# Optimization experiments

Hardware: AMD Instinct MI355X
Metric: run time of the kernel (lower is better)

The kernel has to match this reference:

```python
import jax, jax.numpy as jnp
import numpy as np
import itertools
from jax import lax

B, F, T = 4096, 10, 480
NW, W = 24, 20          # 24 windows of width 20 (index_list = [0,20,...,480])
HID = 64                 # GRU hidden size
NLAYERS = 2
PAIRS = np.array(list(itertools.combinations(range(F), 2)))  # [45,2]
P = PAIRS.shape[0]
D_IN = 2 * P + 12 * F    # GRU input size = 210
BN_EPS = 1e-5


def setup_inputs() -> dict:
    key = jax.random.key(0)
    ks = jax.random.split(key, 16)
    s = 0.1
    g = 1.0 / np.sqrt(HID)
    inp = {
        "data": jax.random.normal(ks[0], (B, 1, F, T), jnp.float32),
        "conv_w": 1.0 + s * jax.random.normal(ks[1], (), jnp.float32),
        "conv_b": s * jax.random.normal(ks[2], (), jnp.float32),
        "bn_gamma": 1.0 + s * jax.random.normal(ks[3], (14,), jnp.float32),
        "bn_beta": s * jax.random.normal(ks[4], (14,), jnp.float32),
        "gru_Wih0": g * jax.random.normal(ks[5], (3 * HID, D_IN), jnp.float32),
        "gru_Whh0": g * jax.random.normal(ks[6], (3 * HID, HID), jnp.float32),
        "gru_bih0": g * jax.random.normal(ks[7], (3 * HID,), jnp.float32),
        "gru_bhh0": g * jax.random.normal(ks[8], (3 * HID,), jnp.float32),
        "gru_Wih1": g * jax.random.normal(ks[9], (3 * HID, HID), jnp.float32),
        "gru_Whh1": g * jax.random.normal(ks[10], (3 * HID, HID), jnp.float32),
        "gru_bih1": g * jax.random.normal(ks[11], (3 * HID,), jnp.float32),
        "gru_bhh1": g * jax.random.normal(ks[12], (3 * HID,), jnp.float32),
        "comb_a": jnp.asarray(PAIRS[:, 0], jnp.int32),
        "comb_b": jnp.asarray(PAIRS[:, 1], jnp.int32),
    }
    return inp


def _gru_layer(x_seq, Wih, Whh, bih, bhh):
    # x_seq: [B, S, D]
    b = x_seq.shape[0]
    h0 = jnp.zeros((b, HID), x_seq.dtype)

    def step(h, xt):
        gi = xt @ Wih.T + bih           # [B, 3H]
        gh = h @ Whh.T + bhh
        i_r, i_z, i_n = jnp.split(gi, 3, axis=-1)
        h_r, h_z, h_n = jnp.split(gh, 3, axis=-1)
        r = jax.nn.sigmoid(i_r + h_r)
        z = jax.nn.sigmoid(i_z + h_z)
        n = jnp.tanh(i_n + r * h_n)
        h_new = (1.0 - z) * n + z * h
        return h_new, h_new

    hT, ys = lax.scan(step, h0, jnp.swapaxes(x_seq, 0, 1))
    return jnp.swapaxes(ys, 0, 1), hT


def reference(data, conv_w, conv_b, bn_gamma, bn_beta,
              gru_Wih0, gru_Whh0, gru_bih0, gru_bhh0,
              gru_Wih1, gru_Whh1, gru_bih1, gru_bhh1,
              comb_a, comb_b):
    b = data.shape[0]
    # uniform index_list -> reshape time into [NW, W] windows
    x = data[:, 0].reshape(b, F, NW, W)            # [B, F, NW, W]
    mean = x.mean(-1)                              # [B, F, NW]
    cen = x - mean[..., None]
    var = (cen * cen).mean(-1)                     # population var (np.std default)
    std = jnp.sqrt(var)
    m3 = (cen ** 3).mean(-1)
    m4 = (cen ** 4).mean(-1)

    # pairwise cov / corr over feature combinations
    xa = x[:, comb_a]                              # [B, P, NW, W]
    xb = x[:, comb_b]
    ca = xa - mean[:, comb_a][..., None]
    cb = xb - mean[:, comb_b][..., None]
    cov = (ca * cb).sum(-1) / (W - 1)              # [B, P, NW]
    corr = cov / (std[:, comb_a] * std[:, comb_b] + 0.01)

    dec_w = (jnp.arange(1, W + 1, dtype=x.dtype) / (W * (W + 1) / 2.0))
    stats = [
        corr,                                      # 1 ts_corr
        cov,                                       # 2 ts_cov
        std,                                       # 3 ts_stddev
        mean / (std + 0.01),                       # 4 ts_zscore
        x[..., -1] / (x[..., 0] + 0.01) - 1.0,     # 5 ts_return
        (x * dec_w).sum(-1),                       # 6 ts_decaylinear
        mean,                                      # 7 ts_mean
        x.min(-1),                                 # 8 ts_min
        var,                                       # 9 ts_var
        x.sum(-1),                                 # 10 ts_sum
        jnp.median(x, axis=-1),                    # 11 ts_median
        m3 / (std ** 3 + 0.01),                    # 12 ts_skew
        m4 / (std ** 4 + 0.01) - 3.0,              # 13 ts_kurtosis
        x.sum(-1),                                 # 14 ts_sum (again)
    ]

    # 1x1 conv (scalar affine, shared) + per-stat BatchNorm2d(1) in training mode
    outs = []
    for i, s_ in enumerate(stats):
        y = conv_w * s_ + conv_b
        m = y.mean()
        v = y.var()
        outs.append(bn_gamma[i] * (y - m) * lax.rsqrt(v + BN_EPS) + bn_beta[i])
    feat = jnp.concatenate(outs, axis=1)           # [B, D_IN, NW]
    seq = jnp.swapaxes(feat, 1, 2)                 # [B, NW, D_IN]

    ys0, _ = _gru_layer(seq, gru_Wih0, gru_Whh0, gru_bih0, gru_bhh0)
    _, h1 = _gru_layer(ys0, gru_Wih1, gru_Whh1, gru_bih1, gru_bhh1)
    return h1                                      # [B, HID]
```

## Files before the change

kernel.cpp:

```cpp
#include <hip/hip_runtime.h>
#include <math.h>

#define NF 10
#define TLEN 480
#define NWIN 24
#define WLEN 20
#define HID 64
#define NPAIR 45
#define DIN 210
#define NG 14
#define GATES 192
#define NGRP 256
#define FROW 212
#define XROW 484
#define NW1 16384
#define NW2 16384

typedef __attribute__((ext_vector_type(8))) short bf16x8;
typedef __attribute__((ext_vector_type(4))) float f32x4;

#define MFMA(a,b,c) __builtin_amdgcn_mfma_f32_16x16x32_bf16((a),(b),(c),0,0,0)

__device__ __forceinline__ int grp_of(int k){ return (k < 90) ? (k / 45) : 2 + (k - 90) / 10; }

__device__ __forceinline__ void split2(float x, short& hi, short& lo){
    unsigned u = __float_as_uint(x);
    hi = (short)(u >> 16);
    float hf = __uint_as_float(u & 0xffff0000u);
    lo = (short)(__float_as_uint(x - hf) >> 16);
}
__device__ __forceinline__ short bf16rne(float x){
    unsigned u = __float_as_uint(x);
    u += 0x7fffu + ((u >> 16) & 1u);
    return (short)(u >> 16);
}
__device__ __forceinline__ float sigm(float x){
    return __builtin_amdgcn_rcpf(1.f + __builtin_amdgcn_exp2f(x * -1.4426950408889634f));
}
__device__ __forceinline__ float tanhfast(float x){
    return 1.f - 2.f * __builtin_amdgcn_rcpf(1.f + __builtin_amdgcn_exp2f(x * 2.8853900817779268f));
}

__global__ __launch_bounds__(256)
void stats_kernel(const float* __restrict__ data, float* __restrict__ feat32,
                  float* __restrict__ part1, float* __restrict__ part2)
{
    __shared__ __align__(16) float xs[NF * XROW];
    __shared__ float ts[NWIN][121];
    __shared__ float tpdot[NWIN][48];
    __shared__ int ca_s[NPAIR], cb_s[NPAIR];
    int b = blockIdx.x, tid = threadIdx.x;
    const float* src = data + (size_t)b * (NF * TLEN);

    for (int q = tid; q < 1200; q += 256){
        int f = q / 120, r = q % 120;
        *(float4*)&xs[f * XROW + r * 4] = *(const float4*)&src[q * 4];
    }
    if (tid < NPAIR){
        int fa = 0, rem = tid;
        while (rem >= 9 - fa){ rem -= (9 - fa); ++fa; }
        ca_s[tid] = fa; cb_s[tid] = fa + 1 + rem;
    }
    __syncthreads();

    float val[12];
    #pragma unroll
    for (int j = 0; j < 12; ++j) val[j] = 0.f;

    if (tid < 240){
        int f = tid / NWIN, t = tid % NWIN;
        const float* p = &xs[f * XROW + t * WLEN];
        float v[WLEN];
        {
            float4 a0 = *(const float4*)(p + 0);
            float4 a1 = *(const float4*)(p + 4);
            float4 a2 = *(const float4*)(p + 8);
            float4 a3 = *(const float4*)(p + 12);
            float4 a4 = *(const float4*)(p + 16);
            v[0]=a0.x; v[1]=a0.y; v[2]=a0.z; v[3]=a0.w;
            v[4]=a1.x; v[5]=a1.y; v[6]=a1.z; v[7]=a1.w;
            v[8]=a2.x; v[9]=a2.y; v[10]=a2.z; v[11]=a2.w;
            v[12]=a3.x; v[13]=a3.y; v[14]=a3.z; v[15]=a3.w;
            v[16]=a4.x; v[17]=a4.y; v[18]=a4.z; v[19]=a4.w;
        }
        float sum = 0.f, wsum = 0.f;
        #pragma unroll
        for (int i = 0; i < WLEN; ++i){
            sum += v[i];
            wsum += v[i] * ((float)(i + 1) * (1.0f / 210.0f));
        }
        float mean = sum * (1.0f / WLEN);
        float var = 0.f, m3 = 0.f, m4 = 0.f;
        #pragma unroll
        for (int i = 0; i < WLEN; ++i){
            float c = v[i] - mean, c2 = c * c;
            var += c2; m3 += c2 * c; m4 += c2 * c2;
        }
        var *= 0.05f; m3 *= 0.05f; m4 *= 0.05f;
        float sd = sqrtf(var);
        float ratio = v[WLEN - 1] / (v[0] + 0.01f) - 1.0f;

        #pragma unroll
        for (int rr = 0; rr < 10; ++rr){
            #pragma unroll
            for (int i = (rr & 1); i + 1 < 10; i += 2){
                float lo0 = fminf(v[i], v[i + 1]);
                float hi0 = fmaxf(v[i], v[i + 1]);
                v[i] = lo0; v[i + 1] = hi0;
                float lo1 = fminf(v[10 + i], v[10 + i + 1]);
                float hi1 = fmaxf(v[10 + i], v[10 + i + 1]);
                v[10 + i] = lo1; v[10 + i + 1] = hi1;
            }
        }
        float Lmax = fminf(v[0], v[19]);
        float Hmin = fmaxf(v[0], v[19]);
        #pragma unroll
        for (int i = 1; i < 10; ++i){
            float li = fminf(v[i], v[19 - i]);
            float hi2 = fmaxf(v[i], v[19 - i]);
            Lmax = fmaxf(Lmax, li);
            Hmin = fminf(Hmin, hi2);
        }
        float median = 0.5f * (Lmax + Hmin);
        float minv = fminf(v[0], v[10]);
        float s3 = sd * sd * sd;
        float mos = mean / (sd + 0.01f);
        float skew = m3 / (s3 + 0.01f);
        float kurt = m4 / (s3 * sd + 0.01f) - 3.0f;

        val[0]=sd; val[1]=mos; val[2]=ratio; val[3]=wsum; val[4]=mean; val[5]=minv;
        val[6]=var; val[7]=sum; val[8]=median; val[9]=skew; val[10]=kurt; val[11]=sum;
        #pragma unroll
        for (int j = 0; j < 12; ++j) ts[t][j * 10 + f] = val[j];
    }
    {
        int wid = b * 4 + (tid >> 6);
        int lane = tid & 63;
        #pragma unroll
        for (int j = 0; j < 12; ++j){
            float a = val[j], q = val[j] * val[j];
            #pragma unroll
            for (int m = 1; m < 64; m <<= 1){
                a += __shfl_xor(a, m);
                q += __shfl_xor(q, m);
            }
            if (lane == 0){
                part1[(size_t)(2 * j) * NW1 + wid] = a;
                part1[(size_t)(2 * j + 1) * NW1 + wid] = q;
            }
        }
    }

    {
        int w = tid >> 6, l = tid & 63;
        int f = l & 15, kb = l >> 4;
        #pragma unroll 1
        for (int s = 0; s < 6; ++s){
            int nw = w * 6 + s;
            float vv[8];
            #pragma unroll
            for (int j = 0; j < 8; ++j) vv[j] = 0.f;
            if (f < NF && kb < 3){
                const float* p = &xs[f * XROW + nw * WLEN + kb * 8];
                float4 u0 = *(const float4*)p;
                vv[0] = u0.x; vv[1] = u0.y; vv[2] = u0.z; vv[3] = u0.w;
                if (kb < 2){
                    float4 u1 = *(const float4*)(p + 4);
                    vv[4] = u1.x; vv[5] = u1.y; vv[6] = u1.z; vv[7] = u1.w;
                }
            }
            bf16x8 Fh, Fl;
            #pragma unroll
            for (int j = 0; j < 8; ++j){ short hi, lo; split2(vv[j], hi, lo); Fh[j] = hi; Fl[j] = lo; }
            f32x4 g = {0.f, 0.f, 0.f, 0.f};
            g = MFMA(Fh, Fh, g);
            g = MFMA(Fh, Fl, g);
            g = MFMA(Fl, Fh, g);
            #pragma unroll
            for (int i = 0; i < 4; ++i){
                int fa = kb * 4 + i, fb = f;
                if (fa < fb && fb < NF){
                    int pi = (((19 - fa) * fa) >> 1) + fb - fa - 1;
                    tpdot[nw][pi] = g[i];
                }
            }
        }
    }
    __syncthreads();

    size_t grp = b >> 4, e = b & 15;
    {
        float cs = 0.f, cq = 0.f, vs2 = 0.f, vq = 0.f;
        for (int q = tid; q < NWIN * NPAIR; q += 256){
            int t = q / NPAIR, pi = q % NPAIR;
            int fa = ca_s[pi], fb = cb_s[pi];
            float dot = tpdot[t][pi];
            float ma = ts[t][40 + fa], mb = ts[t][40 + fb];
            float sa = ts[t][0 + fa],  sb = ts[t][0 + fb];
            float cov = (dot - (float)WLEN * ma * mb) * (1.0f / (WLEN - 1));
            float corr = cov / (sa * sb + 0.01f);
            size_t base = ((grp * NWIN + t) * 16 + e) * FROW;
            feat32[base + pi] = corr;
            feat32[base + NPAIR + pi] = cov;
            cs += corr; cq += corr * corr;
            vs2 += cov; vq += cov * cov;
        }
        float acc[4] = {cs, cq, vs2, vq};
        int wid = b * 4 + (tid >> 6);
        int lane = tid & 63;
        #pragma unroll
        for (int j = 0; j < 4; ++j){
            float a = acc[j];
            #pragma unroll
            for (int m = 1; m < 64; m <<= 1) a += __shfl_xor(a, m);
            if (lane == 0) part2[(size_t)j * NW2 + wid] = a;
        }
    }
    for (int q = tid; q < NWIN * 120; q += 256){
        int t = q / 120, c = q % 120;
        size_t base = ((grp * NWIN + t) * 16 + e) * FROW;
        feat32[base + 90 + c] = ts[t][c];
    }
    if (tid < 48){
        int t = tid >> 1;
        size_t base = ((grp * NWIN + t) * 16 + e) * FROW;
        feat32[base + 210 + (tid & 1)] = 0.f;
    }
}

__global__ __launch_bounds__(256)
void reduce_kernel(const float* __restrict__ part1, const float* __restrict__ part2,
                   float* __restrict__ accum)
{
    __shared__ float red[256];
    int j = blockIdx.x;
    int g = j % NG, which = j / NG;
    const float* base; int n;
    if (g < 2){ base = part2 + (size_t)(g * 2 + which) * NW2; n = NW2; }
    else      { base = part1 + (size_t)((g - 2) * 2 + which) * NW1; n = NW1; }
    int tid = threadIdx.x;
    float s = 0.f;
    for (int i = tid; i < n; i += 256) s += base[i];
    red[tid] = s; __syncthreads();
    for (int step = 128; step > 0; step >>= 1){
        if (tid < step) red[tid] += red[tid + step];
        __syncthreads();
    }
    if (tid == 0) accum[which * NG + g] = red[0];
}

__global__ __launch_bounds__(256)
void prep_kernel(const float* __restrict__ Wih0, const float* __restrict__ Whh0,
                 const float* __restrict__ Wih1, const float* __restrict__ Whh1,
                 const float* __restrict__ bih0, const float* __restrict__ accum,
                 const float* __restrict__ conv_w, const float* __restrict__ bn_gamma,
                 const float* __restrict__ bn_beta,
                 short* __restrict__ WHh, short* __restrict__ W0h, float* __restrict__ bf0)
{
    __shared__ float scs[NG], shs[NG];
    int tid = threadIdx.x;
    if (tid < NG){
        float N = (tid < 2) ? 4096.f * NPAIR * NWIN : 4096.f * NF * NWIN;
        float m = accum[tid] / N;
        float v = accum[NG + tid] / N - m * m;
        float cw = conv_w[0];
        float A = bn_gamma[tid] * rsqrtf(cw * cw * v + 1e-5f);
        scs[tid] = A * cw;
        shs[tid] = bn_beta[tid] - A * cw * m;
    }
    __syncthreads();
    const int NH = 3 * 2 * 12 * 64 * 8;
    const int N0 = 7 * 12 * 64 * 8;
    for (int i = blockIdx.x * 256 + tid; i < NH + N0; i += gridDim.x * 256){
        if (i < NH){
            int j = i & 7, lane = (i >> 3) & 63, rest = i >> 9;
            int ct = rest % 12; rest /= 12;
            int ks = rest & 1, m = rest >> 1;
            int gg = ct * 16 + (lane & 15);
            int k = ks * 32 + ((lane >> 4) << 3) + j;
            const float* Wm = (m == 0) ? Whh0 : (m == 1) ? Wih1 : Whh1;
            WHh[i] = bf16rne(Wm[gg * HID + k]);
        } else {
            int e2 = i - NH;
            int j = e2 & 7, lane = (e2 >> 3) & 63, rest = e2 >> 9;
            int ct = rest % 12, ks = rest / 12;
            int gg = ct * 16 + (lane & 15);
            int k = ks * 32 + ((lane >> 4) << 3) + j;
            float v = (k < DIN) ? Wih0[gg * DIN + k] * scs[grp_of(k)] : 0.f;
            W0h[e2] = bf16rne(v);
        }
    }
    if (blockIdx.x == 0 && tid < GATES){
        float s = bih0[tid];
        for (int k = 0; k < DIN; ++k) s += Wih0[tid * DIN + k] * shs[grp_of(k)];
        bf0[tid] = s;
    }
}

__device__ __forceinline__ void stage_fa(short (*fab)[64][8], int tix,
                                         const float* __restrict__ feat32, int ht)
{
    for (int q = ht; q < 448; q += 256){
        int c = q >> 4, e = q & 15;
        float vv[8];
        const float* src = &feat32[((size_t)tix * 16 + e) * FROW + c * 8];
        if (c < 26){
            float4 u0 = *(const float4*)src, u1 = *(const float4*)(src + 4);
            vv[0]=u0.x; vv[1]=u0.y; vv[2]=u0.z; vv[3]=u0.w;
            vv[4]=u1.x; vv[5]=u1.y; vv[6]=u1.z; vv[7]=u1.w;
        } else if (c == 26){
            float4 u0 = *(const float4*)src;
            vv[0]=u0.x; vv[1]=u0.y; vv[2]=u0.z; vv[3]=u0.w;
            vv[4]=0.f; vv[5]=0.f; vv[6]=0.f; vv[7]=0.f;
        } else {
            #pragma unroll
            for (int j = 0; j < 8; ++j) vv[j] = 0.f;
        }
        bf16x8 h8, l8;
        #pragma unroll
        for (int j = 0; j < 8; ++j){ short hi, lo; split2(vv[j], hi, lo); h8[j] = hi; l8[j] = lo; }
        *(bf16x8*)&fab[(c >> 2) * 2 + 0][e + 16 * (c & 3)][0] = h8;
        *(bf16x8*)&fab[(c >> 2) * 2 + 1][e + 16 * (c & 3)][0] = l8;
    }
}

__global__ __launch_bounds__(512, 1)
void rec_kernel(const float* __restrict__ feat32,
                const short* __restrict__ WHh, const short* __restrict__ W0h,
                const float* __restrict__ bf0, const float* __restrict__ bhh0,
                const float* __restrict__ bih1, const float* __restrict__ bhh1,
                float* __restrict__ out)
{
    __shared__ __align__(16) short fa[2][14][64][8];
    __shared__ __align__(16) short hp0[2][2][16][72];
    __shared__ __align__(16) short hp1[2][2][16][72];
    int tid = threadIdx.x;
    int w = tid >> 6, l = tid & 63;
    int lm = l & 15, kb = l >> 4;
    int blk = blockIdx.x;

    for (int i = tid; i < 2 * 2 * 16 * 72; i += 512){
        ((short*)hp0)[i] = 0;
        ((short*)hp1)[i] = 0;
    }
    for (int q = tid; q < 448; q += 512){
        int c = q >> 4, e = q & 15;
        float vv[8];
        const float* src = &feat32[((size_t)(blk * NWIN) * 16 + e) * FROW + c * 8];
        if (c < 26){
            float4 u0 = *(const float4*)src, u1 = *(const float4*)(src + 4);
            vv[0]=u0.x; vv[1]=u0.y; vv[2]=u0.z; vv[3]=u0.w;
            vv[4]=u1.x; vv[5]=u1.y; vv[6]=u1.z; vv[7]=u1.w;
        } else if (c == 26){
            float4 u0 = *(const float4*)src;
            vv[0]=u0.x; vv[1]=u0.y; vv[2]=u0.z; vv[3]=u0.w;
            vv[4]=0.f; vv[5]=0.f; vv[6]=0.f; vv[7]=0.f;
        } else {
            #pragma unroll
            for (int j = 0; j < 8; ++j) vv[j] = 0.f;
        }
        bf16x8 h8, l8;
        #pragma unroll
        for (int j = 0; j < 8; ++j){ short hi, lo; split2(vv[j], hi, lo); h8[j] = hi; l8[j] = lo; }
        *(bf16x8*)&fa[0][(c >> 2) * 2 + 0][e + 16 * (c & 3)][0] = h8;
        *(bf16x8*)&fa[0][(c >> 2) * 2 + 1][e + 16 * (c & 3)][0] = l8;
    }

    if (w < 4){
        int jc = w * 16 + lm;
        bf16x8 WH0_[2][3];
        #pragma unroll
        for (int ks = 0; ks < 2; ++ks)
            #pragma unroll
            for (int ro = 0; ro < 3; ++ro)
                WH0_[ks][ro] = *(const bf16x8*)&WHh[((((0 * 2 + ks) * 12) + (ro * 4 + w)) * 64 + l) * 8];
        bf16x8 W0_[7][3];
        #pragma unroll
        for (int ks = 0; ks < 7; ++ks)
            #pragma unroll
            for (int ro = 0; ro < 3; ++ro)
                W0_[ks][ro] = *(const bf16x8*)&W0h[(((ks * 12) + (ro * 4 + w)) * 64 + l) * 8];

        float cr0 = bf0[jc]       + bhh0[jc];
        float cz0 = bf0[jc + 64]  + bhh0[jc + 64];
        float cin0 = bf0[jc + 128];
        float chn0 = bhh0[jc + 128];
        float h0p[4] = {0.f, 0.f, 0.f, 0.f};

        __syncthreads();
        #pragma unroll 1
        for (int k = 0; k < 25; ++k){
            if (k < 24){
                int rb = (k & 1) ^ 1, wb = k & 1;
                bf16x8 h0h[2], h0l[2];
                #pragma unroll
                for (int ks = 0; ks < 2; ++ks){
                    int off = ks * 32 + kb * 8;
                    h0h[ks] = *(const bf16x8*)&hp0[rb][0][lm][off];
                    h0l[ks] = *(const bf16x8*)&hp0[rb][1][lm][off];
                }
                f32x4 ar0 = {cr0, cr0, cr0, cr0};
                f32x4 az0 = {cz0, cz0, cz0, cz0};
                f32x4 ain0 = {cin0, cin0, cin0, cin0};
                f32x4 ahn0 = {chn0, chn0, chn0, chn0};
                #pragma unroll
                for (int ks = 0; ks < 2; ++ks){
                    ar0 = MFMA(h0h[ks], WH0_[ks][0], ar0);  ar0 = MFMA(h0l[ks], WH0_[ks][0], ar0);
                    az0 = MFMA(h0h[ks], WH0_[ks][1], az0);  az0 = MFMA(h0l[ks], WH0_[ks][1], az0);
                    ahn0 = MFMA(h0h[ks], WH0_[ks][2], ahn0); ahn0 = MFMA(h0l[ks], WH0_[ks][2], ahn0);
                }
                #pragma unroll
                for (int ks = 0; ks < 7; ++ks){
                    bf16x8 Fh = *(const bf16x8*)&fa[k & 1][ks * 2 + 0][l][0];
                    bf16x8 Fl = *(const bf16x8*)&fa[k & 1][ks * 2 + 1][l][0];
                    ar0 = MFMA(Fh, W0_[ks][0], ar0);  ar0 = MFMA(Fl, W0_[ks][0], ar0);
                    az0 = MFMA(Fh, W0_[ks][1], az0);  az0 = MFMA(Fl, W0_[ks][1], az0);
                    ain0 = MFMA(Fh, W0_[ks][2], ain0); ain0 = MFMA(Fl, W0_[ks][2], ain0);
                }
                #pragma unroll
                for (int i = 0; i < 4; ++i){
                    int row = kb * 4 + i;
                    float rg = sigm(ar0[i]);
                    float zg = sigm(az0[i]);
                    float nn = tanhfast(ain0[i] + rg * ahn0[i]);
                    float h = (1.f - zg) * nn + zg * h0p[i];
                    h0p[i] = h;
                    short hi, lo; split2(h, hi, lo);
                    hp0[wb][0][row][jc] = hi;
                    hp0[wb][1][row][jc] = lo;
                }
            }
            __syncthreads();
        }
    } else {
        int w2 = w - 4;
        int jc = w2 * 16 + lm;
        int ht = tid - 256;
        bf16x8 WH1_[2][3], WH2_[2][3];
        #pragma unroll
        for (int ks = 0; ks < 2; ++ks)
            #pragma unroll
            for (int ro = 0; ro < 3; ++ro){
                WH1_[ks][ro] = *(const bf16x8*)&WHh[((((1 * 2 + ks) * 12) + (ro * 4 + w2)) * 64 + l) * 8];
                WH2_[ks][ro] = *(const bf16x8*)&WHh[((((2 * 2 + ks) * 12) + (ro * 4 + w2)) * 64 + l) * 8];
            }
        float cr1 = bih1[jc]      + bhh1[jc];
        float cz1 = bih1[jc + 64] + bhh1[jc + 64];
        float cin1 = bih1[jc + 128];
        float chn1 = bhh1[jc + 128];
        float h1p[4] = {0.f, 0.f, 0.f, 0.f};

        __syncthreads();
        #pragma unroll 1
        for (int k = 0; k < 25; ++k){
            if (k < 23) stage_fa(fa[(k + 1) & 1], blk * NWIN + k + 1, feat32, ht);
            if (k >= 1){
                int t = k - 1;
                int rb0 = t & 1;
                int rh = (k & 1) ^ 1, wh = k & 1;
                bf16x8 n0h[2], n0l[2], h1h[2], h1l[2];
                #pragma unroll
                for (int ks = 0; ks < 2; ++ks){
                    int off = ks * 32 + kb * 8;
                    n0h[ks] = *(const bf16x8*)&hp0[rb0][0][lm][off];
                    n0l[ks] = *(const bf16x8*)&hp0[rb0][1][lm][off];
                    h1h[ks] = *(const bf16x8*)&hp1[rh][0][lm][off];
                    h1l[ks] = *(const bf16x8*)&hp1[rh][1][lm][off];
                }
                f32x4 ar1 = {cr1, cr1, cr1, cr1};
                f32x4 az1 = {cz1, cz1, cz1, cz1};
                f32x4 ain1 = {cin1, cin1, cin1, cin1};
                f32x4 ahn1 = {chn1, chn1, chn1, chn1};
                #pragma unroll
                for (int ks = 0; ks < 2; ++ks){
                    ar1 = MFMA(n0h[ks], WH1_[ks][0], ar1);  ar1 = MFMA(n0l[ks], WH1_[ks][0], ar1);
                    az1 = MFMA(n0h[ks], WH1_[ks][1], az1);  az1 = MFMA(n0l[ks], WH1_[ks][1], az1);
                    ain1 = MFMA(n0h[ks], WH1_[ks][2], ain1); ain1 = MFMA(n0l[ks], WH1_[ks][2], ain1);
                    ar1 = MFMA(h1h[ks], WH2_[ks][0], ar1);  ar1 = MFMA(h1l[ks], WH2_[ks][0], ar1);
                    az1 = MFMA(h1h[ks], WH2_[ks][1], az1);  az1 = MFMA(h1l[ks], WH2_[ks][1], az1);
                    ahn1 = MFMA(h1h[ks], WH2_[ks][2], ahn1); ahn1 = MFMA(h1l[ks], WH2_[ks][2], ahn1);
                }
                #pragma unroll
                for (int i = 0; i < 4; ++i){
                    int row = kb * 4 + i;
                    float rg = sigm(ar1[i]);
                    float zg = sigm(az1[i]);
                    float nn = tanhfast(ain1[i] + rg * ahn1[i]);
                    float h = (1.f - zg) * nn + zg * h1p[i];
                    h1p[i] = h;
                    short hi, lo; split2(h, hi, lo);
                    hp1[wh][0][row][jc] = hi;
                    hp1[wh][1][row][jc] = lo;
                }
            }
            __syncthreads();
        }
        #pragma unroll
        for (int i = 0; i < 4; ++i)
            out[((size_t)(blk * 16) + kb * 4 + i) * HID + jc] = h1p[i];
    }
}

extern "C" void kernel_launch(void* const* d_in, const int* in_sizes, int n_in,
                              void* d_out, int out_size, void* d_ws, size_t ws_size,
                              hipStream_t stream) {
    const float* data     = (const float*)d_in[0];
    const float* conv_w   = (const float*)d_in[1];
    const float* bn_gamma = (const float*)d_in[3];
    const float* bn_beta  = (const float*)d_in[4];
    const float* Wih0     = (const float*)d_in[5];
    const float* Whh0     = (const float*)d_in[6];
    const float* bih0     = (const float*)d_in[7];
    const float* bhh0     = (const float*)d_in[8];
    const float* Wih1     = (const float*)d_in[9];
    const float* Whh1     = (const float*)d_in[10];
    const float* bih1     = (const float*)d_in[11];
    const float* bhh1     = (const float*)d_in[12];
    float* out = (float*)d_out;

    char* ws = (char*)d_ws;
    const size_t feat32_bytes = (size_t)NGRP * NWIN * 16 * FROW * 4;
    const size_t WH_BYTES = 3 * 2 * 12 * 64 * 8 * 2;
    const size_t W0_BYTES = 7 * 12 * 64 * 8 * 2;
    const size_t P1_BYTES = (size_t)24 * NW1 * 4;

    float* feat32 = (float*)ws;
    short* WHh  = (short*)(ws + feat32_bytes);
    short* W0h  = (short*)(ws + feat32_bytes + WH_BYTES);
    float* bf0  = (float*)(ws + feat32_bytes + WH_BYTES + W0_BYTES);
    float* accum = (float*)(ws + feat32_bytes + WH_BYTES + W0_BYTES + 1024);
    float* part1 = (float*)(ws + feat32_bytes + WH_BYTES + W0_BYTES + 2048);
    float* part2 = (float*)(ws + feat32_bytes + WH_BYTES + W0_BYTES + 2048 + P1_BYTES);

    stats_kernel<<<4096, 256, 0, stream>>>(data, feat32, part1, part2);
    reduce_kernel<<<28, 256, 0, stream>>>(part1, part2, accum);
    prep_kernel<<<64, 256, 0, stream>>>(Wih0, Whh0, Wih1, Whh1, bih0, accum,
                                        conv_w, bn_gamma, bn_beta, WHh, W0h, bf0);
    rec_kernel<<<NGRP, 512, 0, stream>>>(feat32, WHh, W0h, bf0,
                                         bhh0, bih1, bhh1, out);
}
```

Before: 142.9 us.

## Fuse correlation epilogue into MFMA loop and compute per-block stat sums from shared memory

The pairwise dot products from the MFMA are turned into cov/corr directly in registers and written to global memory, which drops the tpdot shared buffer, the pair index tables and one barrier. The per-stat BN partial sums no longer use 12 wavefront shuffle reductions of 24 values each. Instead 120 threads sum columns of the shared stats table and combine them with shared atomics, giving one partial per block rather than one per wave, so the reduce kernel reads less data. In exchange the corr/cov global writes become more scattered (only the lanes holding valid pairs write) and shared-memory atomics are added.

```diff
diff --git a/kernel.cpp b/kernel.cpp
--- a/kernel.cpp
+++ b/kernel.cpp
@@ -13,7 +13,7 @@
 #define NGRP 256
 #define FROW 212
 #define XROW 484
-#define NW1 16384
+#define NB 4096
 #define NW2 16384
 
 typedef __attribute__((ext_vector_type(8))) short bf16x8;
@@ -47,8 +47,7 @@
 {
     __shared__ __align__(16) float xs[NF * XROW];
     __shared__ float ts[NWIN][121];
-    __shared__ float tpdot[NWIN][48];
-    __shared__ int ca_s[NPAIR], cb_s[NPAIR];
+    __shared__ float sgs[NG], sgq[NG];
     int b = blockIdx.x, tid = threadIdx.x;
     const float* src = data + (size_t)b * (NF * TLEN);
 
@@ -56,16 +55,8 @@
         int f = q / 120, r = q % 120;
         *(float4*)&xs[f * XROW + r * 4] = *(const float4*)&src[q * 4];
     }
-    if (tid < NPAIR){
-        int fa = 0, rem = tid;
-        while (rem >= 9 - fa){ rem -= (9 - fa); ++fa; }
-        ca_s[tid] = fa; cb_s[tid] = fa + 1 + rem;
-    }
+    if (tid < NG){ sgs[tid] = 0.f; sgq[tid] = 0.f; }
     __syncthreads();
-
-    float val[12];
-    #pragma unroll
-    for (int j = 0; j < 12; ++j) val[j] = 0.f;
 
     if (tid < 240){
         int f = tid / NWIN, t = tid % NWIN;
@@ -128,32 +119,27 @@
         float skew = m3 / (s3 + 0.01f);
         float kurt = m4 / (s3 * sd + 0.01f) - 3.0f;
 
-        val[0]=sd; val[1]=mos; val[2]=ratio; val[3]=wsum; val[4]=mean; val[5]=minv;
-        val[6]=var; val[7]=sum; val[8]=median; val[9]=skew; val[10]=kurt; val[11]=sum;
-        #pragma unroll
-        for (int j = 0; j < 12; ++j) ts[t][j * 10 + f] = val[j];
-    }
-    {
-        int wid = b * 4 + (tid >> 6);
-        int lane = tid & 63;
-        #pragma unroll
-        for (int j = 0; j < 12; ++j){
-            float a = val[j], q = val[j] * val[j];
-            #pragma unroll
-            for (int m = 1; m < 64; m <<= 1){
-                a += __shfl_xor(a, m);
-                q += __shfl_xor(q, m);
-            }
-            if (lane == 0){
-                part1[(size_t)(2 * j) * NW1 + wid] = a;
-                part1[(size_t)(2 * j + 1) * NW1 + wid] = q;
-            }
-        }
-    }
+        ts[t][  0 + f] = sd;
+        ts[t][ 10 + f] = mos;
+        ts[t][ 20 + f] = ratio;
+        ts[t][ 30 + f] = wsum;
+        ts[t][ 40 + f] = mean;
+        ts[t][ 50 + f] = minv;
+        ts[t][ 60 + f] = var;
+        ts[t][ 70 + f] = sum;
+        ts[t][ 80 + f] = median;
+        ts[t][ 90 + f] = skew;
+        ts[t][100 + f] = kurt;
+        ts[t][110 + f] = sum;
+    }
+    __syncthreads();
+
+    size_t grp = b >> 4, e = b & 15;
 
     {
         int w = tid >> 6, l = tid & 63;
         int f = l & 15, kb = l >> 4;
+        float cs = 0.f, cq = 0.f, vs2 = 0.f, vq = 0.f;
         #pragma unroll 1
         for (int s = 0; s < 6; ++s){
             int nw = w * 6 + s;
@@ -176,45 +162,50 @@
             g = MFMA(Fh, Fh, g);
             g = MFMA(Fh, Fl, g);
             g = MFMA(Fl, Fh, g);
+            size_t base = ((grp * NWIN + nw) * 16 + e) * FROW;
             #pragma unroll
             for (int i = 0; i < 4; ++i){
                 int fa = kb * 4 + i, fb = f;
                 if (fa < fb && fb < NF){
+                    float ma = ts[nw][40 + fa], mb = ts[nw][40 + fb];
+                    float sa = ts[nw][0 + fa],  sb = ts[nw][0 + fb];
+                    float cov = (g[i] - (float)WLEN * ma * mb) * (1.0f / (WLEN - 1));
+                    float corr = cov / (sa * sb + 0.01f);
                     int pi = (((19 - fa) * fa) >> 1) + fb - fa - 1;
-                    tpdot[nw][pi] = g[i];
+                    feat32[base + pi] = corr;
+                    feat32[base + NPAIR + pi] = cov;
+                    cs += corr; cq += corr * corr;
+                    vs2 += cov; vq += cov * cov;
                 }
             }
         }
-    }
-    __syncthreads();
-
-    size_t grp = b >> 4, e = b & 15;
-    {
-        float cs = 0.f, cq = 0.f, vs2 = 0.f, vq = 0.f;
-        for (int q = tid; q < NWIN * NPAIR; q += 256){
-            int t = q / NPAIR, pi = q % NPAIR;
-            int fa = ca_s[pi], fb = cb_s[pi];
-            float dot = tpdot[t][pi];
-            float ma = ts[t][40 + fa], mb = ts[t][40 + fb];
-            float sa = ts[t][0 + fa],  sb = ts[t][0 + fb];
-            float cov = (dot - (float)WLEN * ma * mb) * (1.0f / (WLEN - 1));
-            float corr = cov / (sa * sb + 0.01f);
-            size_t base = ((grp * NWIN + t) * 16 + e) * FROW;
-            feat32[base + pi] = corr;
-            feat32[base + NPAIR + pi] = cov;
-            cs += corr; cq += corr * corr;
-            vs2 += cov; vq += cov * cov;
-        }
         float acc[4] = {cs, cq, vs2, vq};
-        int wid = b * 4 + (tid >> 6);
-        int lane = tid & 63;
+        int wid = b * 4 + w;
         #pragma unroll
         for (int j = 0; j < 4; ++j){
             float a = acc[j];
             #pragma unroll
             for (int m = 1; m < 64; m <<= 1) a += __shfl_xor(a, m);
-            if (lane == 0) part2[(size_t)j * NW2 + wid] = a;
-        }
+            if (l == 0) part2[(size_t)j * NW2 + wid] = a;
+        }
+    }
+
+    if (tid < 120){
+        int g = 2 + tid / 10;
+        float s = 0.f, q = 0.f;
+        #pragma unroll
+        for (int t = 0; t < NWIN; ++t){
+            float v = ts[t][tid];
+            s += v; q += v * v;
+        }
+        atomicAdd(&sgs[g], s);
+        atomicAdd(&sgq[g], q);
+    }
+    __syncthreads();
+
+    if (tid < 24){
+        int j = tid >> 1, wh = tid & 1;
+        part1[(size_t)tid * NB + b] = wh ? sgq[2 + j] : sgs[2 + j];
     }
     for (int q = tid; q < NWIN * 120; q += 256){
         int t = q / 120, c = q % 120;
@@ -237,7 +228,7 @@
     int g = j % NG, which = j / NG;
     const float* base; int n;
     if (g < 2){ base = part2 + (size_t)(g * 2 + which) * NW2; n = NW2; }
-    else      { base = part1 + (size_t)((g - 2) * 2 + which) * NW1; n = NW1; }
+    else      { base = part1 + (size_t)((g - 2) * 2 + which) * NB; n = NB; }
     int tid = threadIdx.x;
     float s = 0.f;
     for (int i = tid; i < n; i += 256) s += base[i];
@@ -522,7 +513,7 @@
     const size_t feat32_bytes = (size_t)NGRP * NWIN * 16 * FROW * 4;
     const size_t WH_BYTES = 3 * 2 * 12 * 64 * 8 * 2;
     const size_t W0_BYTES = 7 * 12 * 64 * 8 * 2;
-    const size_t P1_BYTES = (size_t)24 * NW1 * 4;
+    const size_t P1_BYTES = (size_t)24 * NB * 4;
 
     float* feat32 = (float*)ws;
     short* WHh  = (short*)(ws + feat32_bytes);
@@ -532,7 +523,7 @@
     float* part1 = (float*)(ws + feat32_bytes + WH_BYTES + W0_BYTES + 2048);
     float* part2 = (float*)(ws + feat32_bytes + WH_BYTES + W0_BYTES + 2048 + P1_BYTES);
 
-    stats_kernel<<<4096, 256, 0, stream>>>(data, feat32, part1, part2);
+    stats_kernel<<<NB, 256, 0, stream>>>(data, feat32, part1, part2);
     reduce_kernel<<<28, 256, 0, stream>>>(part1, part2, accum);
     prep_kernel<<<64, 256, 0, stream>>>(Wih0, Whh0, Wih1, Whh1, bih0, accum,
                                         conv_w, bn_gamma, bn_beta, WHh, W0h, bf0);
```

Result: faster. 137.3 us (-3.9%).
